# Optimization experiments

Hardware: AMD Instinct MI355X
Metric: run time of the kernel (lower is better)

The kernel has to match this reference:

```python
import jax, jax.numpy as jnp
import numpy as np

B, N, C = 2, 16384, 128
NUM_HEADS, SR, WS = 2, 4, 8
RED = 4
LN_EPS = 1e-5


def setup_inputs() -> dict:
    key = jax.random.key(0)
    ks = jax.random.split(key, 8)
    std = 0.02
    return {
        "x": jax.random.normal(ks[0], (B, N, C), jnp.float32),
        "q_w": jax.random.normal(ks[1], (C, C), jnp.float32) * std,          # (in,out) layout
        "kv_w": jax.random.normal(ks[2], (C, 2 * C), jnp.float32) * std,
        "sr_w": jax.random.normal(ks[3], (SR, SR, C, C), jnp.float32) * np.sqrt(2.0 / (SR * SR * C)),  # HWIO
        "sr_b": jnp.zeros((C,), jnp.float32),
        "ln_g": jnp.ones((C,), jnp.float32),
        "ln_b": jnp.zeros((C,), jnp.float32),
        "proj_w": jax.random.normal(ks[4], (C, C), jnp.float32) * std,
        "proj_b": jnp.zeros((C,), jnp.float32),
        "f1_w": jax.random.normal(ks[5], (2 * C, 2 * C // RED), jnp.float32) * std,
        "f1_b": jnp.zeros((2 * C // RED,), jnp.float32),
        "f2_w": jax.random.normal(ks[6], (2 * C // RED, 2 * C), jnp.float32) * std,
        "f2_b": jnp.zeros((2 * C,), jnp.float32),
        "H": 128,
        "W": 128,
    }


def _window_partition(t, h, w, s):
    # t: (B, h, w, C) -> (B * (h//s) * (w//s), s*s, C)
    b = t.shape[0]
    t = t.reshape(b, h // s, s, w // s, s, C)
    return t.transpose(0, 1, 3, 2, 4, 5).reshape(-1, s * s, C)


def _forward(x, q_w, kv_w, sr_w, sr_b, ln_g, ln_b, proj_w, proj_b,
             f1_w, f1_b, f2_w, f2_b, H, W):
    nh = NUM_HEADS
    hd = C // nh
    scale = hd ** -0.5

    q = x @ q_w                                          # (B, N, C)

    # --- spatial reduction for k/v (Conv2d k=stride=SR + LayerNorm) ---
    xs = x.reshape(B, H, W, C)
    xr = jax.lax.conv_general_dilated(
        xs, sr_w, window_strides=(SR, SR), padding='VALID',
        dimension_numbers=('NHWC', 'HWIO', 'NHWC')) + sr_b
    Hr, Wr = H // SR, W // SR
    xr = xr.reshape(B, Hr * Wr, C)                       # (B, Nk, C)
    mu = xr.mean(-1, keepdims=True)
    var = ((xr - mu) ** 2).mean(-1, keepdims=True)
    xr = (xr - mu) * jax.lax.rsqrt(var + LN_EPS) * ln_g + ln_b

    kv = xr @ kv_w                                       # (B, Nk, 2C)
    k, v = kv[..., :C], kv[..., C:]

    # --- global SR multi-head attention ---
    qh = q.reshape(B, N, nh, hd)
    kh = k.reshape(B, -1, nh, hd)
    vh = v.reshape(B, -1, nh, hd)
    attn = jax.nn.softmax(jnp.einsum('bqhd,bkhd->bhqk', qh, kh) * scale, axis=-1)
    x_global = jnp.einsum('bhqk,bkhd->bqhd', attn, vh).reshape(B, N, C)

    # --- local windowed attention (single-head over full dim, same scale) ---
    wk = WS // SR
    qw = _window_partition(q.reshape(B, H, W, C), H, W, WS)      # (Bnw, WS*WS, C)
    kw = _window_partition(k.reshape(B, Hr, Wr, C), Hr, Wr, wk)  # (Bnw, wk*wk, C)
    vw = _window_partition(v.reshape(B, Hr, Wr, C), Hr, Wr, wk)
    a = jax.nn.softmax(jnp.einsum('wqc,wkc->wqk', qw, kw) * scale, axis=-1)
    xl = jnp.einsum('wqk,wkc->wqc', a, vw)                       # (Bnw, WS*WS, C)
    # window reverse -> (B, N, C)
    xl = xl.reshape(B, H // WS, W // WS, WS, WS, C)
    x_local = xl.transpose(0, 1, 3, 2, 4, 5).reshape(B, N, C)

    # --- InteractiveFusion_C: SE-style cross channel gating (reconstructed) ---
    z = jnp.concatenate([x_global.mean(axis=1), x_local.mean(axis=1)], axis=-1)  # (B, 2C)
    z = jax.nn.sigmoid(jax.nn.relu(z @ f1_w + f1_b) @ f2_w + f2_b)               # (B, 2C)
    gg, gl = z[:, None, :C], z[:, None, C:]
    fused = gg * x_global + gl * x_local                                          # (B, N, C)

    return fused @ proj_w + proj_b


def reference(x, q_w, kv_w, sr_w, sr_b, ln_g, ln_b, proj_w, proj_b,
              f1_w, f1_b, f2_w, f2_b, H, W):
    return _forward(x, q_w, kv_w, sr_w, sr_b, ln_g, ln_b, proj_w, proj_b,
                    f1_w, f1_b, f2_w, f2_b, H, W)
```

## Files before the change

### kernel.cpp

```cpp
#include <hip/hip_runtime.h>
#include <hip/hip_bf16.h>
#include <math.h>

constexpr int kB  = 2;
constexpr int kN  = 16384;
constexpr int kC  = 128;
constexpr int kNr = 1024;
constexpr float kScale = 0.125f;

typedef short bf16x8 __attribute__((ext_vector_type(8)));
typedef float f32x4  __attribute__((ext_vector_type(4)));

__device__ inline ushort f2bf(float x) {
  __hip_bfloat16 h = __float2bfloat16(x);
  return *(ushort*)&h;
}
__device__ inline unsigned pack_bf16(float a, float b) {
  return (unsigned)f2bf(a) | ((unsigned)f2bf(b) << 16);
}
__device__ inline float bf2f(ushort u) {
  unsigned v = ((unsigned)u) << 16;
  return __uint_as_float(v);
}

#define FMA16(ACC, AV, BV)                                                              \
  do {                                                                                  \
    ACC[0][0] += AV.x * BV.x; ACC[0][1] += AV.x * BV.y;                                 \
    ACC[0][2] += AV.x * BV.z; ACC[0][3] += AV.x * BV.w;                                 \
    ACC[1][0] += AV.y * BV.x; ACC[1][1] += AV.y * BV.y;                                 \
    ACC[1][2] += AV.y * BV.z; ACC[1][3] += AV.y * BV.w;                                 \
    ACC[2][0] += AV.z * BV.x; ACC[2][1] += AV.z * BV.y;                                 \
    ACC[2][2] += AV.z * BV.z; ACC[2][3] += AV.z * BV.w;                                 \
    ACC[3][0] += AV.w * BV.x; ACC[3][1] += AV.w * BV.y;                                 \
    ACC[3][2] += AV.w * BV.z; ACC[3][3] += AV.w * BV.w;                                 \
  } while (0)

__global__ __launch_bounds__(256) void zero_kernel(float* p, int n) {
  int i = blockIdx.x * 256 + threadIdx.x;
  if (i < n) p[i] = 0.f;
}

__global__ __launch_bounds__(256) void cast_x(const float* __restrict__ x,
                                              ushort* __restrict__ xbf) {
  int i = (blockIdx.x * 256 + threadIdx.x) * 8;
  float4 a = *(const float4*)&x[i];
  float4 b = *(const float4*)&x[i + 4];
  uint4 o;
  o.x = pack_bf16(a.x, a.y); o.y = pack_bf16(a.z, a.w);
  o.z = pack_bf16(b.x, b.y); o.w = pack_bf16(b.z, b.w);
  *(uint4*)&xbf[i] = o;
}

__global__ __launch_bounds__(256) void transp_bf(const float* __restrict__ w,
                                                 ushort* __restrict__ wt,
                                                 int K, int N) {
  int flat4 = blockIdx.x * 256 + threadIdx.x;
  int n4pr = N >> 2;
  int k = flat4 / n4pr, n = (flat4 % n4pr) * 4;
  if (k >= K) return;
  float4 v = *(const float4*)&w[(size_t)k * N + n];
  wt[(size_t)(n + 0) * K + k] = f2bf(v.x);
  wt[(size_t)(n + 1) * K + k] = f2bf(v.y);
  wt[(size_t)(n + 2) * K + k] = f2bf(v.z);
  wt[(size_t)(n + 3) * K + k] = f2bf(v.w);
}

__global__ __launch_bounds__(256) void gemm_q_mfma(const ushort* __restrict__ xbf,
                                                   const ushort* __restrict__ wt,
                                                   ushort* __restrict__ Cbf) {
  __shared__ __align__(16) char Bs[32768];
  const int t = threadIdx.x, l = t & 63, w = t >> 6, c = l & 15, lg = l >> 4;
  const int m0 = blockIdx.x * 64;
#pragma unroll
  for (int r = 0; r < 8; ++r) {
    int sf = r * 256 + t;
    int n = sf >> 4, sl = sf & 15;
    uint4 v = *(const uint4*)(wt + n * 128 + sl * 8);
    *(uint4*)(Bs + ((n * 256 + sl * 16) ^ ((n & 7) << 4))) = v;
  }
  __syncthreads();
  const int mrow = m0 + 16 * w + c;
  f32x4 acc[8];
#pragma unroll
  for (int i = 0; i < 8; ++i) acc[i] = f32x4{0.f, 0.f, 0.f, 0.f};
#pragma unroll
  for (int ks = 0; ks < 4; ++ks) {
    bf16x8 af = *(const bf16x8*)(xbf + (size_t)mrow * 128 + ks * 32 + 8 * lg);
#pragma unroll
    for (int nt = 0; nt < 8; ++nt) {
      int n = 16 * nt + c;
      bf16x8 bf = *(const bf16x8*)(Bs + ((n * 256 + 64 * ks + 16 * lg) ^ ((n & 7) << 4)));
      acc[nt] = __builtin_amdgcn_mfma_f32_16x16x32_bf16(af, bf, acc[nt], 0, 0, 0);
    }
  }
#pragma unroll
  for (int nt = 0; nt < 8; ++nt) {
    int col = 16 * nt + c;
#pragma unroll
    for (int r = 0; r < 4; ++r)
      Cbf[(size_t)(m0 + 16 * w + 4 * lg + r) * 128 + col] = f2bf(acc[nt][r] * kScale);
  }
}

__global__ __launch_bounds__(256) void conv_mfma(const ushort* __restrict__ xbf,
                                                 const ushort* __restrict__ swt,
                                                 float* __restrict__ xr) {
  const int t = threadIdx.x, l = t & 63, w = t >> 6, c = l & 15, lg = l >> 4;
  const int m0 = blockIdx.x * 16;
  const int n0 = blockIdx.y * 64 + w * 16;
  const int p = m0 + c;
  const int pb_ = p >> 10, hr = (p & 1023) >> 5, wr = p & 31;
  f32x4 acc = {0.f, 0.f, 0.f, 0.f};
  for (int tp = 0; tp < 16; ++tp) {
    int ti = tp >> 2, tj = tp & 3;
    const ushort* ap = xbf + (size_t)((pb_ * 128 + hr * 4 + ti) * 128 + wr * 4 + tj) * 128;
    const ushort* bp = swt + (size_t)(n0 + c) * 2048 + tp * 128;
#pragma unroll
    for (int ks = 0; ks < 4; ++ks) {
      bf16x8 af = *(const bf16x8*)(ap + ks * 32 + 8 * lg);
      bf16x8 bf = *(const bf16x8*)(bp + ks * 32 + 8 * lg);
      acc = __builtin_amdgcn_mfma_f32_16x16x32_bf16(af, bf, acc, 0, 0, 0);
    }
  }
#pragma unroll
  for (int r = 0; r < 4; ++r)
    xr[(size_t)(m0 + 4 * lg + r) * 128 + n0 + c] = acc[r];
}

__global__ __launch_bounds__(256) void ln_kernel(float* __restrict__ xr,
                                                 const float* __restrict__ sb,
                                                 const float* __restrict__ lg,
                                                 const float* __restrict__ lb) {
  int t = threadIdx.x;
  int lane = t & 63, wv = t >> 6;
  int row = blockIdx.x * 4 + wv;
  float2 v = *(float2*)&xr[(size_t)row * 128 + lane * 2];
  v.x += sb[lane * 2]; v.y += sb[lane * 2 + 1];
  float sum = v.x + v.y, sq = v.x * v.x + v.y * v.y;
#pragma unroll
  for (int o = 1; o < 64; o <<= 1) {
    sum += __shfl_xor(sum, o, 64);
    sq  += __shfl_xor(sq, o, 64);
  }
  float mu  = sum * (1.f / 128.f);
  float var = sq * (1.f / 128.f) - mu * mu;
  float inv = 1.0f / sqrtf(var + 1e-5f);
  float2 o2;
  o2.x = (v.x - mu) * inv * lg[lane * 2] + lb[lane * 2];
  o2.y = (v.y - mu) * inv * lg[lane * 2 + 1] + lb[lane * 2 + 1];
  *(float2*)&xr[(size_t)row * 128 + lane * 2] = o2;
}

__global__ __launch_bounds__(256) void gemm_kv(const float* __restrict__ A,
                                               const float* __restrict__ Bm,
                                               float* __restrict__ kvb,
                                               ushort* __restrict__ kbf,
                                               ushort* __restrict__ vtbf) {
  __shared__ float As[32][68];
  __shared__ float Bs[32][68];
  const int t = threadIdx.x, tx = t & 15, ty = t >> 4;
  const int n0 = blockIdx.x * 64, m0 = blockIdx.y * 64;
  float acc[4][4] = {};
  for (int k0 = 0; k0 < 128; k0 += 32) {
#pragma unroll
    for (int r = 0; r < 2; ++r) {
      int flat = r * 256 + t;
      int m = flat >> 3, kg = (flat & 7) * 4;
      float4 a4 = *(const float4*)&A[(size_t)(m0 + m) * 128 + k0 + kg];
      As[kg + 0][m] = a4.x; As[kg + 1][m] = a4.y;
      As[kg + 2][m] = a4.z; As[kg + 3][m] = a4.w;
      int kk = flat >> 4, ng = (flat & 15) * 4;
      *(float4*)&Bs[kk][ng] = *(const float4*)&Bm[(size_t)(k0 + kk) * 256 + n0 + ng];
    }
    __syncthreads();
#pragma unroll
    for (int k = 0; k < 32; ++k) {
      float4 av = *(const float4*)&As[k][ty * 4];
      float4 bv = *(const float4*)&Bs[k][tx * 4];
      FMA16(acc, av, bv);
    }
    __syncthreads();
  }
#pragma unroll
  for (int i = 0; i < 4; ++i) {
    int m = m0 + ty * 4 + i;
    int b = m >> 10, tok = m & 1023;
    float4 o = make_float4(acc[i][0], acc[i][1], acc[i][2], acc[i][3]);
    *(float4*)&kvb[(size_t)m * 256 + n0 + tx * 4] = o;
#pragma unroll
    for (int j = 0; j < 4; ++j) {
      int n = n0 + tx * 4 + j;
      float val = acc[i][j];
      if (n < 128) {
        int h = n >> 6, dl = n & 63;
        kbf[((size_t)((b * 2 + h) * 1024 + tok)) * 64 + dl] = f2bf(val);
      } else {
        int d = n - 128, h = d >> 6, dl = d & 63;
        vtbf[((size_t)((b * 2 + h) * 64 + dl)) * 1024 + tok] = f2bf(val);
      }
    }
  }
}

__global__ __launch_bounds__(256) void attn_mfma(const ushort* __restrict__ qbf,
                                                 const ushort* __restrict__ kbf,
                                                 const ushort* __restrict__ vtbf,
                                                 ushort* __restrict__ xgbf) {
  __shared__ __align__(16) char sm[49152];
  const int t = threadIdx.x;
  const int l = t & 63, w = t >> 6;
  const int c = l & 15, lg = l >> 4;
  const int h = blockIdx.y, b = blockIdx.z;
  const int qb = blockIdx.x * 128;
  char* Pw = sm + 32768 + w * 4096;
  const size_t bh = (size_t)(b * 2 + h);

  const int f0 = t, f1 = 256 + t;
  const int kk0 = f0 >> 3, sl0 = f0 & 7, kk1 = f1 >> 3, sl1 = f1 & 7;
  const int d0 = (kk0 * 128 + sl0 * 16) ^ ((kk0 & 7) << 4);
  const int d1 = (kk1 * 128 + sl1 * 16) ^ ((kk1 & 7) << 4);
  const ushort* ksrc0 = kbf + (bh * 1024 + kk0) * 64 + sl0 * 8;
  const ushort* ksrc1 = kbf + (bh * 1024 + kk1) * 64 + sl1 * 8;
  const ushort* vsrc0 = vtbf + (bh * 64 + kk0) * 1024 + sl0 * 8;
  const ushort* vsrc1 = vtbf + (bh * 64 + kk1) * 1024 + sl1 * 8;

  bf16x8 qf[2][2];
#pragma unroll
  for (int n = 0; n < 2; ++n)
#pragma unroll
    for (int f = 0; f < 2; ++f) {
      size_t off = ((size_t)(b * kN + qb + 32 * w + 16 * n + c)) * 128
                   + h * 64 + 32 * f + 8 * lg;
      qf[n][f] = *(const bf16x8*)(qbf + off);
    }

  float l_run[2] = {0.f, 0.f};
  f32x4 o[2][4] = {};

  {
    uint4 k0 = *(const uint4*)ksrc0;
    uint4 k1 = *(const uint4*)ksrc1;
    uint4 v0 = *(const uint4*)vsrc0;
    uint4 v1 = *(const uint4*)vsrc1;
    *(uint4*)(sm + d0) = k0;        *(uint4*)(sm + d1) = k1;
    *(uint4*)(sm + 8192 + d0) = v0; *(uint4*)(sm + 8192 + d1) = v1;
  }
  __syncthreads();

  int cur = 0;
  for (int cc = 0; cc < 16; ++cc) {
    char* Kb = sm + cur * 16384;
    char* Vb = Kb + 8192;
    uint4 nk0, nk1, nv0, nv1;
    if (cc < 15) {
      nk0 = *(const uint4*)(ksrc0 + (cc + 1) * 4096);
      nk1 = *(const uint4*)(ksrc1 + (cc + 1) * 4096);
      nv0 = *(const uint4*)(vsrc0 + (cc + 1) * 64);
      nv1 = *(const uint4*)(vsrc1 + (cc + 1) * 64);
    }

    bf16x8 kf[4][2];
#pragma unroll
    for (int kt = 0; kt < 4; ++kt)
#pragma unroll
      for (int f = 0; f < 2; ++f) {
        int row = kt * 16 + c;
        kf[kt][f] = *(const bf16x8*)(Kb + ((row * 128 + 64 * f + 16 * lg)
                                           ^ ((row & 7) << 4)));
      }

#pragma unroll
    for (int n = 0; n < 2; ++n) {
      f32x4 s4[4];
#pragma unroll
      for (int kt = 0; kt < 4; ++kt) {
        f32x4 z = {0.f, 0.f, 0.f, 0.f};
        z = __builtin_amdgcn_mfma_f32_16x16x32_bf16(kf[kt][0], qf[n][0], z, 0, 0, 0);
        s4[kt] = __builtin_amdgcn_mfma_f32_16x16x32_bf16(kf[kt][1], qf[n][1], z, 0, 0, 0);
      }
      float psum = 0.f;
#pragma unroll
      for (int kt = 0; kt < 4; ++kt)
#pragma unroll
        for (int r = 0; r < 4; ++r) {
          float p = __expf(s4[kt][r]);
          s4[kt][r] = p; psum += p;
        }
      psum += __shfl_xor(psum, 16, 64);
      psum += __shfl_xor(psum, 32, 64);
      l_run[n] += psum;
      int qq = 16 * n + c;
#pragma unroll
      for (int kt = 0; kt < 4; ++kt) {
        uint2 pk2;
        pk2.x = pack_bf16(s4[kt][0], s4[kt][1]);
        pk2.y = pack_bf16(s4[kt][2], s4[kt][3]);
        *(uint2*)(Pw + ((qq * 128 + 32 * kt + 8 * lg) ^ ((qq & 7) << 4))) = pk2;
      }
    }

    bf16x8 pf[2][2];
#pragma unroll
    for (int n = 0; n < 2; ++n)
#pragma unroll
      for (int hh = 0; hh < 2; ++hh) {
        int qq = 16 * n + c;
        pf[n][hh] = *(const bf16x8*)(Pw + ((qq * 128 + 64 * hh + 16 * lg)
                                           ^ ((qq & 7) << 4)));
      }
#pragma unroll
    for (int dt = 0; dt < 4; ++dt) {
      bf16x8 vf[2];
#pragma unroll
      for (int hh = 0; hh < 2; ++hh) {
        int row = 16 * dt + c;
        vf[hh] = *(const bf16x8*)(Vb + ((row * 128 + 64 * hh + 16 * lg)
                                        ^ ((row & 7) << 4)));
      }
#pragma unroll
      for (int n = 0; n < 2; ++n) {
        f32x4 acc = o[n][dt];
        acc = __builtin_amdgcn_mfma_f32_16x16x32_bf16(pf[n][0], vf[0], acc, 0, 0, 0);
        o[n][dt] = __builtin_amdgcn_mfma_f32_16x16x32_bf16(pf[n][1], vf[1], acc, 0, 0, 0);
      }
    }

    if (cc < 15) {
      char* Kn = sm + (cur ^ 1) * 16384;
      char* Vn = Kn + 8192;
      *(uint4*)(Kn + d0) = nk0; *(uint4*)(Kn + d1) = nk1;
      *(uint4*)(Vn + d0) = nv0; *(uint4*)(Vn + d1) = nv1;
    }
    __syncthreads();
    cur ^= 1;
  }

#pragma unroll
  for (int n = 0; n < 2; ++n) {
    float i0 = 1.f / __shfl(l_run[n], 4 * lg + 0, 64);
    float i1 = 1.f / __shfl(l_run[n], 4 * lg + 1, 64);
    float i2 = 1.f / __shfl(l_run[n], 4 * lg + 2, 64);
    float i3 = 1.f / __shfl(l_run[n], 4 * lg + 3, 64);
#pragma unroll
    for (int dt = 0; dt < 4; ++dt) {
      int dg = h * 64 + 16 * dt + c;
      size_t base = ((size_t)(b * kN + qb + 32 * w + 16 * n + 4 * lg)) * 128 + dg;
      xgbf[base]       = f2bf(o[n][dt][0] * i0);
      xgbf[base + 128] = f2bf(o[n][dt][1] * i1);
      xgbf[base + 256] = f2bf(o[n][dt][2] * i2);
      xgbf[base + 384] = f2bf(o[n][dt][3] * i3);
    }
  }
}

__global__ __launch_bounds__(256) void local_attn(const ushort* __restrict__ qbf,
                                                  const float* __restrict__ kv,
                                                  ushort* __restrict__ xlbf) {
  __shared__ float Qw[64][132];
  __shared__ float Kw[4][132];
  __shared__ float Vw[4][132];
  __shared__ float Pw[64][4];
  const int t = threadIdx.x;
  const int wi = blockIdx.x;
  const int b = wi >> 8, wrem = wi & 255, wy = wrem >> 4, wx = wrem & 15;

#pragma unroll
  for (int r = 0; r < 4; ++r) {
    int flat = r * 256 + t;
    int tok = flat >> 4, g8 = (flat & 15) * 8;
    int sy = tok >> 3, sx = tok & 7;
    int n = (wy * 8 + sy) * 128 + wx * 8 + sx;
    uint4 v = *(const uint4*)(qbf + ((size_t)(b * kN + n)) * 128 + g8);
    ushort* us = (ushort*)&v;
    Qw[tok][g8 + 0] = bf2f(us[0]); Qw[tok][g8 + 1] = bf2f(us[1]);
    Qw[tok][g8 + 2] = bf2f(us[2]); Qw[tok][g8 + 3] = bf2f(us[3]);
    Qw[tok][g8 + 4] = bf2f(us[4]); Qw[tok][g8 + 5] = bf2f(us[5]);
    Qw[tok][g8 + 6] = bf2f(us[6]); Qw[tok][g8 + 7] = bf2f(us[7]);
  }
  {
    int half = t >> 7, tt = t & 127;
    int tok = tt >> 5, g = (tt & 31) * 4;
    int sy = tok >> 1, sx = tok & 1;
    int kr = (wy * 2 + sy) * 32 + wx * 2 + sx;
    float4 v4 = *(const float4*)&kv[((size_t)(b * kNr + kr)) * 256 + half * 128 + g];
    if (half == 0) *(float4*)&Kw[tok][g] = v4;
    else           *(float4*)&Vw[tok][g] = v4;
  }
  __syncthreads();

  {
    int r = t >> 2, kk = t & 3;
    float s = 0.f;
#pragma unroll
    for (int g = 0; g < 128; g += 4) {
      float4 a  = *(const float4*)&Qw[r][g];
      float4 bb = *(const float4*)&Kw[kk][g];
      s += a.x * bb.x + a.y * bb.y + a.z * bb.z + a.w * bb.w;
    }
    float m = s;
    m = fmaxf(m, __shfl_xor(m, 1, 64));
    m = fmaxf(m, __shfl_xor(m, 2, 64));
    float e = __expf(s - m);
    float sum = e;
    sum += __shfl_xor(sum, 1, 64);
    sum += __shfl_xor(sum, 2, 64);
    Pw[r][kk] = e / sum;
  }
  __syncthreads();

  {
    int r = t >> 2, cg = (t & 3) * 32;
    float p0 = Pw[r][0], p1 = Pw[r][1], p2 = Pw[r][2], p3 = Pw[r][3];
    int sy = r >> 3, sx = r & 7;
    int n = (wy * 8 + sy) * 128 + wx * 8 + sx;
    ushort* dst = &xlbf[((size_t)(b * kN + n)) * 128 + cg];
#pragma unroll
    for (int g = 0; g < 32; g += 4) {
      float4 v0 = *(const float4*)&Vw[0][cg + g];
      float4 v1 = *(const float4*)&Vw[1][cg + g];
      float4 v2 = *(const float4*)&Vw[2][cg + g];
      float4 v3 = *(const float4*)&Vw[3][cg + g];
      float ox = p0 * v0.x + p1 * v1.x + p2 * v2.x + p3 * v3.x;
      float oy = p0 * v0.y + p1 * v1.y + p2 * v2.y + p3 * v3.y;
      float oz = p0 * v0.z + p1 * v1.z + p2 * v2.z + p3 * v3.z;
      float ow = p0 * v0.w + p1 * v1.w + p2 * v2.w + p3 * v3.w;
      uint2 pk;
      pk.x = pack_bf16(ox, oy); pk.y = pack_bf16(oz, ow);
      *(uint2*)&dst[g] = pk;
    }
  }
}

__global__ __launch_bounds__(256) void colmean(const ushort* __restrict__ xgbf,
                                               const ushort* __restrict__ xlbf,
                                               float* __restrict__ zsums) {
  __shared__ float bg[16][128], bl[16][128];
  int b = blockIdx.y, t = threadIdx.x;
  int cg = (t & 15) * 8, stripe = t >> 4;
  int r0 = blockIdx.x * 256 + stripe * 16;
  float sg[8] = {}, sl[8] = {};
  for (int i = 0; i < 16; ++i) {
    size_t base = ((size_t)(b * kN + r0 + i)) * 128 + cg;
    uint4 g = *(const uint4*)(xgbf + base);
    uint4 lv = *(const uint4*)(xlbf + base);
    ushort* gu = (ushort*)&g; ushort* lu = (ushort*)&lv;
#pragma unroll
    for (int j = 0; j < 8; ++j) {
      sg[j] += bf2f(gu[j]);
      sl[j] += bf2f(lu[j]);
    }
  }
#pragma unroll
  for (int j = 0; j < 8; ++j) {
    bg[stripe][cg + j] = sg[j];
    bl[stripe][cg + j] = sl[j];
  }
  __syncthreads();
  if (t < 128) {
    float s = 0.f;
#pragma unroll
    for (int st = 0; st < 16; ++st) s += bg[st][t];
    atomicAdd(&zsums[b * 256 + t], s);
  } else {
    int col = t - 128;
    float s = 0.f;
#pragma unroll
    for (int st = 0; st < 16; ++st) s += bl[st][col];
    atomicAdd(&zsums[b * 256 + 128 + col], s);
  }
}

__global__ __launch_bounds__(256) void gate_mlp(const float* __restrict__ zsums,
                                                const float* __restrict__ f1w,
                                                const float* __restrict__ f1b,
                                                const float* __restrict__ f2w,
                                                const float* __restrict__ f2b,
                                                float* __restrict__ gates) {
  __shared__ float z[256];
  __shared__ float hbuf[64];
  int b = blockIdx.x, t = threadIdx.x;
  z[t] = zsums[b * 256 + t] * (1.0f / 16384.0f);
  __syncthreads();
  if (t < 64) {
    float a = f1b[t];
    for (int j = 0; j < 256; ++j) a += z[j] * f1w[j * 64 + t];
    hbuf[t] = fmaxf(a, 0.f);
  }
  __syncthreads();
  {
    float a = f2b[t];
    for (int j = 0; j < 64; ++j) a += hbuf[j] * f2w[j * 256 + t];
    gates[b * 256 + t] = 1.f / (1.f + __expf(-a));
  }
}

__global__ __launch_bounds__(256) void fused_proj_mfma(const ushort* __restrict__ xgbf,
                                                       const ushort* __restrict__ xlbf,
                                                       const float* __restrict__ gates,
                                                       const ushort* __restrict__ pwt,
                                                       const float* __restrict__ pb,
                                                       float* __restrict__ out) {
  __shared__ __align__(16) char Bs[32768];
  __shared__ float Gg[128], Gl[128];
  const int t = threadIdx.x, l = t & 63, w = t >> 6, c = l & 15, lg = l >> 4;
  const int m0 = blockIdx.x * 64;
  const int b = m0 >> 14;
#pragma unroll
  for (int r = 0; r < 8; ++r) {
    int sf = r * 256 + t;
    int n = sf >> 4, sl = sf & 15;
    uint4 v = *(const uint4*)(pwt + n * 128 + sl * 8);
    *(uint4*)(Bs + ((n * 256 + sl * 16) ^ ((n & 7) << 4))) = v;
  }
  if (t < 128) Gg[t] = gates[b * 256 + t];
  else         Gl[t - 128] = gates[b * 256 + t];
  __syncthreads();
  const int mrow = m0 + 16 * w + c;
  f32x4 acc[8];
#pragma unroll
  for (int i = 0; i < 8; ++i) acc[i] = f32x4{0.f, 0.f, 0.f, 0.f};
#pragma unroll
  for (int ks = 0; ks < 4; ++ks) {
    int k8 = ks * 32 + 8 * lg;
    uint4 gv = *(const uint4*)(xgbf + (size_t)mrow * 128 + k8);
    uint4 lv = *(const uint4*)(xlbf + (size_t)mrow * 128 + k8);
    ushort* gu = (ushort*)&gv; ushort* lu = (ushort*)&lv;
    float f[8];
#pragma unroll
    for (int j = 0; j < 8; ++j)
      f[j] = Gg[k8 + j] * bf2f(gu[j]) + Gl[k8 + j] * bf2f(lu[j]);
    union { bf16x8 v; unsigned u[4]; } au;
    au.u[0] = pack_bf16(f[0], f[1]); au.u[1] = pack_bf16(f[2], f[3]);
    au.u[2] = pack_bf16(f[4], f[5]); au.u[3] = pack_bf16(f[6], f[7]);
#pragma unroll
    for (int nt = 0; nt < 8; ++nt) {
      int n = 16 * nt + c;
      bf16x8 bf = *(const bf16x8*)(Bs + ((n * 256 + 64 * ks + 16 * lg) ^ ((n & 7) << 4)));
      acc[nt] = __builtin_amdgcn_mfma_f32_16x16x32_bf16(au.v, bf, acc[nt], 0, 0, 0);
    }
  }
#pragma unroll
  for (int nt = 0; nt < 8; ++nt) {
    int col = 16 * nt + c;
    float bias = pb[col];
#pragma unroll
    for (int r = 0; r < 4; ++r)
      out[(size_t)(m0 + 16 * w + 4 * lg + r) * 128 + col] = acc[nt][r] + bias;
  }
}

extern "C" void kernel_launch(void* const* d_in, const int* in_sizes, int n_in,
                              void* d_out, int out_size, void* d_ws, size_t ws_size,
                              hipStream_t stream) {
  const float* x      = (const float*)d_in[0];
  const float* q_w    = (const float*)d_in[1];
  const float* kv_w   = (const float*)d_in[2];
  const float* sr_w   = (const float*)d_in[3];
  const float* sr_b   = (const float*)d_in[4];
  const float* ln_g   = (const float*)d_in[5];
  const float* ln_b   = (const float*)d_in[6];
  const float* proj_w = (const float*)d_in[7];
  const float* proj_b = (const float*)d_in[8];
  const float* f1_w   = (const float*)d_in[9];
  const float* f1_b   = (const float*)d_in[10];
  const float* f2_w   = (const float*)d_in[11];
  const float* f2_b   = (const float*)d_in[12];
  float* out = (float*)d_out;

  float* ws = (float*)d_ws;
  float* kvb   = ws;
  float* xr    = kvb + 524288;
  float* zsums = xr + 262144;
  float* gates = zsums + 512;
  ushort* xbf  = (ushort*)(gates + 512);
  ushort* qbf  = xbf + 4194304;
  ushort* kbf  = qbf + 4194304;
  ushort* vtbf = kbf + 262144;
  ushort* xgbf = vtbf + 262144;
  ushort* xlbf = xgbf + 4194304;
  ushort* qwt  = xlbf + 4194304;
  ushort* pwt  = qwt + 16384;
  ushort* swt  = pwt + 16384;

  zero_kernel<<<dim3(2), 256, 0, stream>>>(zsums, 512);

  cast_x<<<dim3(2048), 256, 0, stream>>>(x, xbf);
  transp_bf<<<dim3(16), 256, 0, stream>>>(q_w, qwt, 128, 128);
  transp_bf<<<dim3(16), 256, 0, stream>>>(proj_w, pwt, 128, 128);
  transp_bf<<<dim3(256), 256, 0, stream>>>(sr_w, swt, 2048, 128);

  gemm_q_mfma<<<dim3(512), 256, 0, stream>>>(xbf, qwt, qbf);
  conv_mfma<<<dim3(128, 2), 256, 0, stream>>>(xbf, swt, xr);
  ln_kernel<<<dim3(512), 256, 0, stream>>>(xr, sr_b, ln_g, ln_b);
  gemm_kv<<<dim3(4, 32), 256, 0, stream>>>(xr, kv_w, kvb, kbf, vtbf);
  attn_mfma<<<dim3(128, 2, 2), 256, 0, stream>>>(qbf, kbf, vtbf, xgbf);
  local_attn<<<dim3(512), 256, 0, stream>>>(qbf, kvb, xlbf);
  colmean<<<dim3(64, 2), 256, 0, stream>>>(xgbf, xlbf, zsums);
  gate_mlp<<<dim3(2), 256, 0, stream>>>(zsums, f1_w, f1_b, f2_w, f2_b, gates);
  fused_proj_mfma<<<dim3(512), 256, 0, stream>>>(xgbf, xlbf, gates, pwt, proj_b, out);
}
```

Measured before the change: 196.5 us.

## Fuse conv+LN+KV GEMM, merge prep kernels, fold column means into attention

Merges the cast, weight transposes and zeroing into one prep launch. Fuses the strided conv, LayerNorm and the KV projection into a single MFMA kernel that writes bf16 K/V directly, replacing the fp32 SIMT GEMM and its intermediate buffers. Removes the separate colmean pass by accumulating column sums inside global attention and computing local-window means algebraically from the softmax weights and V. This cuts launches and a full re-read of the two large bf16 outputs, at the cost of more atomics and a conv kernel with fewer blocks.

```diff
diff --git a/kernel.cpp b/kernel.cpp
--- a/kernel.cpp
+++ b/kernel.cpp
@@ -23,38 +23,9 @@
   return __uint_as_float(v);
 }
 
-#define FMA16(ACC, AV, BV)                                                              \
-  do {                                                                                  \
-    ACC[0][0] += AV.x * BV.x; ACC[0][1] += AV.x * BV.y;                                 \
-    ACC[0][2] += AV.x * BV.z; ACC[0][3] += AV.x * BV.w;                                 \
-    ACC[1][0] += AV.y * BV.x; ACC[1][1] += AV.y * BV.y;                                 \
-    ACC[1][2] += AV.y * BV.z; ACC[1][3] += AV.y * BV.w;                                 \
-    ACC[2][0] += AV.z * BV.x; ACC[2][1] += AV.z * BV.y;                                 \
-    ACC[2][2] += AV.z * BV.z; ACC[2][3] += AV.z * BV.w;                                 \
-    ACC[3][0] += AV.w * BV.x; ACC[3][1] += AV.w * BV.y;                                 \
-    ACC[3][2] += AV.w * BV.z; ACC[3][3] += AV.w * BV.w;                                 \
-  } while (0)
-
-__global__ __launch_bounds__(256) void zero_kernel(float* p, int n) {
-  int i = blockIdx.x * 256 + threadIdx.x;
-  if (i < n) p[i] = 0.f;
-}
-
-__global__ __launch_bounds__(256) void cast_x(const float* __restrict__ x,
-                                              ushort* __restrict__ xbf) {
-  int i = (blockIdx.x * 256 + threadIdx.x) * 8;
-  float4 a = *(const float4*)&x[i];
-  float4 b = *(const float4*)&x[i + 4];
-  uint4 o;
-  o.x = pack_bf16(a.x, a.y); o.y = pack_bf16(a.z, a.w);
-  o.z = pack_bf16(b.x, b.y); o.w = pack_bf16(b.z, b.w);
-  *(uint4*)&xbf[i] = o;
-}
-
-__global__ __launch_bounds__(256) void transp_bf(const float* __restrict__ w,
-                                                 ushort* __restrict__ wt,
-                                                 int K, int N) {
-  int flat4 = blockIdx.x * 256 + threadIdx.x;
+__device__ inline void transp_body(const float* __restrict__ w,
+                                   ushort* __restrict__ wt,
+                                   int K, int N, int flat4) {
   int n4pr = N >> 2;
   int k = flat4 / n4pr, n = (flat4 % n4pr) * 4;
   if (k >= K) return;
@@ -65,6 +36,40 @@
   wt[(size_t)(n + 3) * K + k] = f2bf(v.w);
 }
 
+__global__ __launch_bounds__(256) void prep(const float* __restrict__ x,
+                                            const float* __restrict__ q_w,
+                                            const float* __restrict__ proj_w,
+                                            const float* __restrict__ kv_w,
+                                            const float* __restrict__ sr_w,
+                                            ushort* __restrict__ xbf,
+                                            ushort* __restrict__ qwt,
+                                            ushort* __restrict__ pwt,
+                                            ushort* __restrict__ kwt,
+                                            ushort* __restrict__ swt,
+                                            float* __restrict__ zsums) {
+  int bid = blockIdx.x, t = threadIdx.x;
+  if (bid < 2048) {
+    int i = (bid * 256 + t) * 8;
+    float4 a = *(const float4*)&x[i];
+    float4 b = *(const float4*)&x[i + 4];
+    uint4 o;
+    o.x = pack_bf16(a.x, a.y); o.y = pack_bf16(a.z, a.w);
+    o.z = pack_bf16(b.x, b.y); o.w = pack_bf16(b.z, b.w);
+    *(uint4*)&xbf[i] = o;
+  } else if (bid < 2064) {
+    transp_body(q_w, qwt, 128, 128, (bid - 2048) * 256 + t);
+  } else if (bid < 2080) {
+    transp_body(proj_w, pwt, 128, 128, (bid - 2064) * 256 + t);
+  } else if (bid < 2112) {
+    transp_body(kv_w, kwt, 128, 256, (bid - 2080) * 256 + t);
+  } else if (bid < 2368) {
+    transp_body(sr_w, swt, 2048, 128, (bid - 2112) * 256 + t);
+  } else {
+    zsums[t] = 0.f;
+    zsums[256 + t] = 0.f;
+  }
+}
+
 __global__ __launch_bounds__(256) void gemm_q_mfma(const ushort* __restrict__ xbf,
                                                    const ushort* __restrict__ wt,
                                                    ushort* __restrict__ Cbf) {
@@ -102,110 +107,115 @@
   }
 }
 
-__global__ __launch_bounds__(256) void conv_mfma(const ushort* __restrict__ xbf,
-                                                 const ushort* __restrict__ swt,
-                                                 float* __restrict__ xr) {
+__global__ __launch_bounds__(256) void convlnkv(const ushort* __restrict__ xbf,
+                                                const ushort* __restrict__ swt,
+                                                const float* __restrict__ sr_b,
+                                                const float* __restrict__ ln_g,
+                                                const float* __restrict__ ln_b,
+                                                const ushort* __restrict__ kwt,
+                                                ushort* __restrict__ kbf,
+                                                ushort* __restrict__ vtbf,
+                                                ushort* __restrict__ vbf) {
+  __shared__ float Lf[16][132];
+  __shared__ __align__(16) char Lbf[4096];
   const int t = threadIdx.x, l = t & 63, w = t >> 6, c = l & 15, lg = l >> 4;
   const int m0 = blockIdx.x * 16;
-  const int n0 = blockIdx.y * 64 + w * 16;
   const int p = m0 + c;
   const int pb_ = p >> 10, hr = (p & 1023) >> 5, wr = p & 31;
-  f32x4 acc = {0.f, 0.f, 0.f, 0.f};
+
+  f32x4 acc[2];
+  acc[0] = f32x4{0.f, 0.f, 0.f, 0.f};
+  acc[1] = f32x4{0.f, 0.f, 0.f, 0.f};
   for (int tp = 0; tp < 16; ++tp) {
     int ti = tp >> 2, tj = tp & 3;
-    const ushort* ap = xbf + (size_t)((pb_ * 128 + hr * 4 + ti) * 128 + wr * 4 + tj) * 128;
-    const ushort* bp = swt + (size_t)(n0 + c) * 2048 + tp * 128;
+    const ushort* ap =
+        xbf + (size_t)((pb_ * 128 + hr * 4 + ti) * 128 + wr * 4 + tj) * 128;
 #pragma unroll
     for (int ks = 0; ks < 4; ++ks) {
       bf16x8 af = *(const bf16x8*)(ap + ks * 32 + 8 * lg);
-      bf16x8 bf = *(const bf16x8*)(bp + ks * 32 + 8 * lg);
-      acc = __builtin_amdgcn_mfma_f32_16x16x32_bf16(af, bf, acc, 0, 0, 0);
-    }
-  }
-#pragma unroll
-  for (int r = 0; r < 4; ++r)
-    xr[(size_t)(m0 + 4 * lg + r) * 128 + n0 + c] = acc[r];
-}
-
-__global__ __launch_bounds__(256) void ln_kernel(float* __restrict__ xr,
-                                                 const float* __restrict__ sb,
-                                                 const float* __restrict__ lg,
-                                                 const float* __restrict__ lb) {
-  int t = threadIdx.x;
-  int lane = t & 63, wv = t >> 6;
-  int row = blockIdx.x * 4 + wv;
-  float2 v = *(float2*)&xr[(size_t)row * 128 + lane * 2];
-  v.x += sb[lane * 2]; v.y += sb[lane * 2 + 1];
-  float sum = v.x + v.y, sq = v.x * v.x + v.y * v.y;
-#pragma unroll
-  for (int o = 1; o < 64; o <<= 1) {
-    sum += __shfl_xor(sum, o, 64);
-    sq  += __shfl_xor(sq, o, 64);
-  }
-  float mu  = sum * (1.f / 128.f);
-  float var = sq * (1.f / 128.f) - mu * mu;
-  float inv = 1.0f / sqrtf(var + 1e-5f);
-  float2 o2;
-  o2.x = (v.x - mu) * inv * lg[lane * 2] + lb[lane * 2];
-  o2.y = (v.y - mu) * inv * lg[lane * 2 + 1] + lb[lane * 2 + 1];
-  *(float2*)&xr[(size_t)row * 128 + lane * 2] = o2;
-}
-
-__global__ __launch_bounds__(256) void gemm_kv(const float* __restrict__ A,
-                                               const float* __restrict__ Bm,
-                                               float* __restrict__ kvb,
-                                               ushort* __restrict__ kbf,
-                                               ushort* __restrict__ vtbf) {
-  __shared__ float As[32][68];
-  __shared__ float Bs[32][68];
-  const int t = threadIdx.x, tx = t & 15, ty = t >> 4;
-  const int n0 = blockIdx.x * 64, m0 = blockIdx.y * 64;
-  float acc[4][4] = {};
-  for (int k0 = 0; k0 < 128; k0 += 32) {
-#pragma unroll
-    for (int r = 0; r < 2; ++r) {
-      int flat = r * 256 + t;
-      int m = flat >> 3, kg = (flat & 7) * 4;
-      float4 a4 = *(const float4*)&A[(size_t)(m0 + m) * 128 + k0 + kg];
-      As[kg + 0][m] = a4.x; As[kg + 1][m] = a4.y;
-      As[kg + 2][m] = a4.z; As[kg + 3][m] = a4.w;
-      int kk = flat >> 4, ng = (flat & 15) * 4;
-      *(float4*)&Bs[kk][ng] = *(const float4*)&Bm[(size_t)(k0 + kk) * 256 + n0 + ng];
-    }
-    __syncthreads();
-#pragma unroll
-    for (int k = 0; k < 32; ++k) {
-      float4 av = *(const float4*)&As[k][ty * 4];
-      float4 bv = *(const float4*)&Bs[k][tx * 4];
-      FMA16(acc, av, bv);
-    }
-    __syncthreads();
-  }
-#pragma unroll
-  for (int i = 0; i < 4; ++i) {
-    int m = m0 + ty * 4 + i;
-    int b = m >> 10, tok = m & 1023;
-    float4 o = make_float4(acc[i][0], acc[i][1], acc[i][2], acc[i][3]);
-    *(float4*)&kvb[(size_t)m * 256 + n0 + tx * 4] = o;
-#pragma unroll
-    for (int j = 0; j < 4; ++j) {
-      int n = n0 + tx * 4 + j;
-      float val = acc[i][j];
+#pragma unroll
+      for (int nt = 0; nt < 2; ++nt) {
+        int n = w * 32 + 16 * nt + c;
+        bf16x8 bf = *(const bf16x8*)(swt + (size_t)n * 2048 + tp * 128 + ks * 32 + 8 * lg);
+        acc[nt] = __builtin_amdgcn_mfma_f32_16x16x32_bf16(af, bf, acc[nt], 0, 0, 0);
+      }
+    }
+  }
+#pragma unroll
+  for (int nt = 0; nt < 2; ++nt)
+#pragma unroll
+    for (int r = 0; r < 4; ++r) {
+      int col = w * 32 + 16 * nt + c;
+      Lf[4 * lg + r][col] = acc[nt][r] + sr_b[col];
+    }
+  __syncthreads();
+
+  {
+    int row = t >> 4, c8 = (t & 15) * 8;
+    float v[8];
+    float s = 0.f, sq = 0.f;
+#pragma unroll
+    for (int j = 0; j < 8; ++j) {
+      v[j] = Lf[row][c8 + j];
+      s += v[j]; sq += v[j] * v[j];
+    }
+#pragma unroll
+    for (int off = 1; off < 16; off <<= 1) {
+      s  += __shfl_xor(s, off, 64);
+      sq += __shfl_xor(sq, off, 64);
+    }
+    float mu  = s * (1.f / 128.f);
+    float var = sq * (1.f / 128.f) - mu * mu;
+    float inv = 1.0f / sqrtf(var + 1e-5f);
+    uint4 pk;
+    unsigned* pu = (unsigned*)&pk;
+#pragma unroll
+    for (int j2 = 0; j2 < 4; ++j2) {
+      float a = (v[2 * j2]     - mu) * inv * ln_g[c8 + 2 * j2]     + ln_b[c8 + 2 * j2];
+      float b = (v[2 * j2 + 1] - mu) * inv * ln_g[c8 + 2 * j2 + 1] + ln_b[c8 + 2 * j2 + 1];
+      pu[j2] = pack_bf16(a, b);
+    }
+    *(uint4*)(Lbf + ((row * 256 + c8 * 2) ^ ((row & 7) << 4))) = pk;
+  }
+  __syncthreads();
+
+  f32x4 a2[4];
+#pragma unroll
+  for (int i = 0; i < 4; ++i) a2[i] = f32x4{0.f, 0.f, 0.f, 0.f};
+#pragma unroll
+  for (int ks = 0; ks < 4; ++ks) {
+    bf16x8 af = *(const bf16x8*)(Lbf + ((c * 256 + ks * 64 + 16 * lg) ^ ((c & 7) << 4)));
+#pragma unroll
+    for (int nt = 0; nt < 4; ++nt) {
+      int n = w * 64 + 16 * nt + c;
+      bf16x8 bf = *(const bf16x8*)(kwt + (size_t)n * 128 + ks * 32 + 8 * lg);
+      a2[nt] = __builtin_amdgcn_mfma_f32_16x16x32_bf16(af, bf, a2[nt], 0, 0, 0);
+    }
+  }
+#pragma unroll
+  for (int nt = 0; nt < 4; ++nt)
+#pragma unroll
+    for (int r = 0; r < 4; ++r) {
+      int m = m0 + 4 * lg + r;
+      int b = m >> 10, tok = m & 1023;
+      int n = w * 64 + 16 * nt + c;
+      ushort val = f2bf(a2[nt][r]);
       if (n < 128) {
         int h = n >> 6, dl = n & 63;
-        kbf[((size_t)((b * 2 + h) * 1024 + tok)) * 64 + dl] = f2bf(val);
+        kbf[((size_t)((b * 2 + h) * 1024 + tok)) * 64 + dl] = val;
       } else {
         int d = n - 128, h = d >> 6, dl = d & 63;
-        vtbf[((size_t)((b * 2 + h) * 64 + dl)) * 1024 + tok] = f2bf(val);
-      }
-    }
-  }
+        vbf[((size_t)((b * 2 + h) * 1024 + tok)) * 64 + dl] = val;
+        vtbf[((size_t)((b * 2 + h) * 64 + dl)) * 1024 + tok] = val;
+      }
+    }
 }
 
 __global__ __launch_bounds__(256) void attn_mfma(const ushort* __restrict__ qbf,
                                                  const ushort* __restrict__ kbf,
                                                  const ushort* __restrict__ vtbf,
-                                                 ushort* __restrict__ xgbf) {
+                                                 ushort* __restrict__ xgbf,
+                                                 float* __restrict__ zsums) {
   __shared__ __align__(16) char sm[49152];
   const int t = threadIdx.x;
   const int l = t & 63, w = t >> 6;
@@ -335,6 +345,7 @@
     cur ^= 1;
   }
 
+  float cs[4] = {0.f, 0.f, 0.f, 0.f};
 #pragma unroll
   for (int n = 0; n < 2; ++n) {
     float i0 = 1.f / __shfl(l_run[n], 4 * lg + 0, 64);
@@ -343,24 +354,46 @@
     float i3 = 1.f / __shfl(l_run[n], 4 * lg + 3, 64);
 #pragma unroll
     for (int dt = 0; dt < 4; ++dt) {
+      float v0 = o[n][dt][0] * i0, v1 = o[n][dt][1] * i1;
+      float v2 = o[n][dt][2] * i2, v3 = o[n][dt][3] * i3;
       int dg = h * 64 + 16 * dt + c;
       size_t base = ((size_t)(b * kN + qb + 32 * w + 16 * n + 4 * lg)) * 128 + dg;
-      xgbf[base]       = f2bf(o[n][dt][0] * i0);
-      xgbf[base + 128] = f2bf(o[n][dt][1] * i1);
-      xgbf[base + 256] = f2bf(o[n][dt][2] * i2);
-      xgbf[base + 384] = f2bf(o[n][dt][3] * i3);
-    }
+      xgbf[base]       = f2bf(v0);
+      xgbf[base + 128] = f2bf(v1);
+      xgbf[base + 256] = f2bf(v2);
+      xgbf[base + 384] = f2bf(v3);
+      cs[dt] += v0 + v1 + v2 + v3;
+    }
+  }
+#pragma unroll
+  for (int dt = 0; dt < 4; ++dt) {
+    cs[dt] += __shfl_xor(cs[dt], 16, 64);
+    cs[dt] += __shfl_xor(cs[dt], 32, 64);
+  }
+  float* Cs = (float*)sm;
+  if (l < 16) {
+#pragma unroll
+    for (int dt = 0; dt < 4; ++dt) Cs[w * 64 + dt * 16 + l] = cs[dt];
+  }
+  __syncthreads();
+  if (t < 64) {
+    float s = Cs[t] + Cs[64 + t] + Cs[128 + t] + Cs[192 + t];
+    atomicAdd(&zsums[b * 256 + h * 64 + t], s);
   }
 }
 
 __global__ __launch_bounds__(256) void local_attn(const ushort* __restrict__ qbf,
-                                                  const float* __restrict__ kv,
-                                                  ushort* __restrict__ xlbf) {
+                                                  const ushort* __restrict__ kbf,
+                                                  const ushort* __restrict__ vbf,
+                                                  ushort* __restrict__ xlbf,
+                                                  float* __restrict__ zsums) {
   __shared__ float Qw[64][132];
   __shared__ float Kw[4][132];
   __shared__ float Vw[4][132];
   __shared__ float Pw[64][4];
+  __shared__ float cwp[4][4];
   const int t = threadIdx.x;
+  const int l = t & 63, w = t >> 6;
   const int wi = blockIdx.x;
   const int b = wi >> 8, wrem = wi & 255, wy = wrem >> 4, wx = wrem & 15;
 
@@ -382,9 +415,13 @@
     int tok = tt >> 5, g = (tt & 31) * 4;
     int sy = tok >> 1, sx = tok & 1;
     int kr = (wy * 2 + sy) * 32 + wx * 2 + sx;
-    float4 v4 = *(const float4*)&kv[((size_t)(b * kNr + kr)) * 256 + half * 128 + g];
-    if (half == 0) *(float4*)&Kw[tok][g] = v4;
-    else           *(float4*)&Vw[tok][g] = v4;
+    int h = g >> 6, dl = g & 63;
+    const ushort* src = (half ? vbf : kbf) + ((size_t)((b * 2 + h) * 1024 + kr)) * 64 + dl;
+    uint2 v2 = *(const uint2*)src;
+    ushort* us = (ushort*)&v2;
+    float4 f = make_float4(bf2f(us[0]), bf2f(us[1]), bf2f(us[2]), bf2f(us[3]));
+    if (half == 0) *(float4*)&Kw[tok][g] = f;
+    else           *(float4*)&Vw[tok][g] = f;
   }
   __syncthreads();
 
@@ -407,6 +444,15 @@
     Pw[r][kk] = e / sum;
   }
   __syncthreads();
+
+  {
+    float pv = Pw[t >> 2][t & 3];
+    pv += __shfl_xor(pv, 4, 64);
+    pv += __shfl_xor(pv, 8, 64);
+    pv += __shfl_xor(pv, 16, 64);
+    pv += __shfl_xor(pv, 32, 64);
+    if (l < 4) cwp[w][l] = pv;
+  }
 
   {
     int r = t >> 2, cg = (t & 3) * 32;
@@ -429,44 +475,15 @@
       *(uint2*)&dst[g] = pk;
     }
   }
-}
-
-__global__ __launch_bounds__(256) void colmean(const ushort* __restrict__ xgbf,
-                                               const ushort* __restrict__ xlbf,
-                                               float* __restrict__ zsums) {
-  __shared__ float bg[16][128], bl[16][128];
-  int b = blockIdx.y, t = threadIdx.x;
-  int cg = (t & 15) * 8, stripe = t >> 4;
-  int r0 = blockIdx.x * 256 + stripe * 16;
-  float sg[8] = {}, sl[8] = {};
-  for (int i = 0; i < 16; ++i) {
-    size_t base = ((size_t)(b * kN + r0 + i)) * 128 + cg;
-    uint4 g = *(const uint4*)(xgbf + base);
-    uint4 lv = *(const uint4*)(xlbf + base);
-    ushort* gu = (ushort*)&g; ushort* lu = (ushort*)&lv;
-#pragma unroll
-    for (int j = 0; j < 8; ++j) {
-      sg[j] += bf2f(gu[j]);
-      sl[j] += bf2f(lu[j]);
-    }
-  }
-#pragma unroll
-  for (int j = 0; j < 8; ++j) {
-    bg[stripe][cg + j] = sg[j];
-    bl[stripe][cg + j] = sl[j];
-  }
-  __syncthreads();
+  __syncthreads();
+
   if (t < 128) {
-    float s = 0.f;
-#pragma unroll
-    for (int st = 0; st < 16; ++st) s += bg[st][t];
-    atomicAdd(&zsums[b * 256 + t], s);
-  } else {
-    int col = t - 128;
-    float s = 0.f;
-#pragma unroll
-    for (int st = 0; st < 16; ++st) s += bl[st][col];
-    atomicAdd(&zsums[b * 256 + 128 + col], s);
+    float p0 = cwp[0][0] + cwp[1][0] + cwp[2][0] + cwp[3][0];
+    float p1 = cwp[0][1] + cwp[1][1] + cwp[2][1] + cwp[3][1];
+    float p2 = cwp[0][2] + cwp[1][2] + cwp[2][2] + cwp[3][2];
+    float p3 = cwp[0][3] + cwp[1][3] + cwp[2][3] + cwp[3][3];
+    float s = p0 * Vw[0][t] + p1 * Vw[1][t] + p2 * Vw[2][t] + p3 * Vw[3][t];
+    atomicAdd(&zsums[b * 256 + 128 + t], s);
   }
 }
 
@@ -568,34 +585,27 @@
   float* out = (float*)d_out;
 
   float* ws = (float*)d_ws;
-  float* kvb   = ws;
-  float* xr    = kvb + 524288;
-  float* zsums = xr + 262144;
+  float* zsums = ws;
   float* gates = zsums + 512;
   ushort* xbf  = (ushort*)(gates + 512);
   ushort* qbf  = xbf + 4194304;
   ushort* kbf  = qbf + 4194304;
   ushort* vtbf = kbf + 262144;
-  ushort* xgbf = vtbf + 262144;
+  ushort* vbf  = vtbf + 262144;
+  ushort* xgbf = vbf + 262144;
   ushort* xlbf = xgbf + 4194304;
   ushort* qwt  = xlbf + 4194304;
   ushort* pwt  = qwt + 16384;
-  ushort* swt  = pwt + 16384;
-
-  zero_kernel<<<dim3(2), 256, 0, stream>>>(zsums, 512);
-
-  cast_x<<<dim3(2048), 256, 0, stream>>>(x, xbf);
-  transp_bf<<<dim3(16), 256, 0, stream>>>(q_w, qwt, 128, 128);
-  transp_bf<<<dim3(16), 256, 0, stream>>>(proj_w, pwt, 128, 128);
-  transp_bf<<<dim3(256), 256, 0, stream>>>(sr_w, swt, 2048, 128);
-
+  ushort* kwt  = pwt + 16384;
+  ushort* swt  = kwt + 32768;
+
+  prep<<<dim3(2369), 256, 0, stream>>>(x, q_w, proj_w, kv_w, sr_w,
+                                       xbf, qwt, pwt, kwt, swt, zsums);
   gemm_q_mfma<<<dim3(512), 256, 0, stream>>>(xbf, qwt, qbf);
-  conv_mfma<<<dim3(128, 2), 256, 0, stream>>>(xbf, swt, xr);
-  ln_kernel<<<dim3(512), 256, 0, stream>>>(xr, sr_b, ln_g, ln_b);
-  gemm_kv<<<dim3(4, 32), 256, 0, stream>>>(xr, kv_w, kvb, kbf, vtbf);
-  attn_mfma<<<dim3(128, 2, 2), 256, 0, stream>>>(qbf, kbf, vtbf, xgbf);
-  local_attn<<<dim3(512), 256, 0, stream>>>(qbf, kvb, xlbf);
-  colmean<<<dim3(64, 2), 256, 0, stream>>>(xgbf, xlbf, zsums);
+  convlnkv<<<dim3(128), 256, 0, stream>>>(xbf, swt, sr_b, ln_g, ln_b, kwt,
+                                          kbf, vtbf, vbf);
+  attn_mfma<<<dim3(128, 2, 2), 256, 0, stream>>>(qbf, kbf, vtbf, xgbf, zsums);
+  local_attn<<<dim3(512), 256, 0, stream>>>(qbf, kbf, vbf, xlbf, zsums);
   gate_mlp<<<dim3(2), 256, 0, stream>>>(zsums, f1_w, f1_b, f2_w, f2_b, gates);
   fused_proj_mfma<<<dim3(512), 256, 0, stream>>>(xgbf, xlbf, gates, pwt, proj_b, out);
 }
```

After: 197.4 us. Within noise of the previous version (+0.5%).
